# Kernel optimization log

Hardware: AMD Instinct MI355X
Metric: run time of the kernel (lower is better)

The kernel has to match this reference:

```python
import jax, jax.numpy as jnp
import numpy as np

B, D, C = 32768, 1024, 40  # batch, proj_dim, num_classes('culture')


def setup_inputs() -> dict:
    key = jax.random.key(0)
    k1, k2, k3, k4, k5 = jax.random.split(key, 5)
    scale = 1.0 / np.sqrt(D)
    return {
        "src": jax.random.normal(k1, (B, D), dtype=jnp.float32),
        "attn_mask": jnp.ones((B,), dtype=jnp.float32),  # unpacked but unused by BiChain
        # padded weights: row i uses only first D+i columns; the rest hit zero buffer slots
        "W": jax.random.normal(k2, (C, D + C), dtype=jnp.float32) * scale,
        "b": jax.random.normal(k3, (C,), dtype=jnp.float32) * scale,
        "W_rev": jax.random.normal(k4, (C, D + C), dtype=jnp.float32) * scale,
        "b_rev": jax.random.normal(k5, (C,), dtype=jnp.float32) * scale,
    }


def _chain(src, W, b):
    """Sequential classifier chain: score_i = sigmoid(<[src, s_0..s_{i-1}], w_i> + b_i)."""
    Bsz, Df = src.shape
    Cn = W.shape[0]
    # growing feature buffer, pre-padded with zeros for future scores
    buf0 = jnp.zeros((Bsz, Df + Cn), dtype=src.dtype).at[:, :Df].set(src)

    def step(buf, inp):
        w_i, b_i, i = inp
        score = jax.nn.sigmoid(buf @ w_i + b_i)            # [B]
        buf = jax.lax.dynamic_update_slice(buf, score[:, None], (0, Df + i))
        return buf, score

    _, scores = jax.lax.scan(step, buf0, (W, b, jnp.arange(Cn)))
    return scores.T  # [B, C]


def reference(src, attn_mask, W, b, W_rev, b_rev):
    out_fwd = _chain(src, W, b)
    out_rev = _chain(src, W_rev, b_rev)
    return (out_fwd + out_rev[:, ::-1]) * 0.5
```

## Files before the change

kernel.cpp:

```cpp
#include <hip/hip_runtime.h>
#include <hip/hip_bf16.h>
#include <math.h>

using short8   = __attribute__((ext_vector_type(8))) short;
using ushort4v = __attribute__((ext_vector_type(4))) unsigned short;
using float4v  = __attribute__((ext_vector_type(4))) float;

#define D_DIM 1024
#define NCLS  40
#define WSTR  1064
#define TM    64
#define NCH   16

__device__ __forceinline__ short f2bf(float f) {
    __hip_bfloat16 h = __float2bfloat16(f);
    union { __hip_bfloat16 h; short s; } u; u.h = h;
    return u.s;
}

__global__ void convert_w_kernel(const float* __restrict__ W, const float* __restrict__ Wr,
                                 short* __restrict__ Wfrag) {
    int idx  = blockIdx.x * 256 + threadIdx.x;
    int lane = idx & 63;
    int rest = idx >> 6;
    int t    = rest % 5;
    int rest2 = rest / 5;
    int ks   = rest2 & 1;
    int ch   = rest2 >> 1;
    int cls  = t * 16 + (lane & 15);
    int k0   = ch * 64 + ks * 32 + (lane >> 4) * 8;
    const float* srow = (cls < NCLS) ? (W + (size_t)cls * WSTR)
                                     : (Wr + (size_t)(cls - NCLS) * WSTR);
    short8 v;
#pragma unroll
    for (int e = 0; e < 8; ++e) v[e] = f2bf(srow[k0 + e]);
    *(short8*)(Wfrag + (size_t)idx * 8) = v;
}

__global__ __launch_bounds__(256, 2) void bichain_main(
    const float* __restrict__ src, const short* __restrict__ Wfrag,
    const float* __restrict__ Wf, const float* __restrict__ Wr,
    const float* __restrict__ bf_, const float* __restrict__ br_,
    float* __restrict__ out)
{
    __shared__ __align__(16) char smem[24576];

    const int tid  = threadIdx.x;
    const int lane = tid & 63;
    const int wave = tid >> 6;
    const int row0 = blockIdx.x * TM;
    const int i16  = lane & 15;
    const int i4   = lane >> 4;

    char* ldsW = smem + wave * 6144;
    const float* aGlob = src + (size_t)(row0 + wave * 16 + i4) * D_DIM + i16 * 4;

    float4v ap[3][4];
    short8  wp[2][10];
    float4v acc[5];
#pragma unroll
    for (int t = 0; t < 5; ++t)
#pragma unroll
        for (int r = 0; r < 4; ++r) acc[t][r] = 0.f;

#define LOADA(ch) do { if ((ch) < NCH) {                                   \
    const float* _p = aGlob + (ch) * 64;                                   \
    ap[(ch)%3][0] = *(const float4v*)(_p);                                 \
    ap[(ch)%3][1] = *(const float4v*)(_p + 4 * D_DIM);                     \
    ap[(ch)%3][2] = *(const float4v*)(_p + 8 * D_DIM);                     \
    ap[(ch)%3][3] = *(const float4v*)(_p + 12 * D_DIM); } } while (0)

#define LOADW(ch) do { if ((ch) < NCH) {                                   \
    const short* _w = Wfrag + (size_t)(ch) * 5120 + (lane << 3);           \
    wp[(ch)%2][0] = *(const short8*)(_w + 0 * 512);                        \
    wp[(ch)%2][1] = *(const short8*)(_w + 1 * 512);                        \
    wp[(ch)%2][2] = *(const short8*)(_w + 2 * 512);                        \
    wp[(ch)%2][3] = *(const short8*)(_w + 3 * 512);                        \
    wp[(ch)%2][4] = *(const short8*)(_w + 4 * 512);                        \
    wp[(ch)%2][5] = *(const short8*)(_w + 5 * 512);                        \
    wp[(ch)%2][6] = *(const short8*)(_w + 6 * 512);                        \
    wp[(ch)%2][7] = *(const short8*)(_w + 7 * 512);                        \
    wp[(ch)%2][8] = *(const short8*)(_w + 8 * 512);                        \
    wp[(ch)%2][9] = *(const short8*)(_w + 9 * 512); } } while (0)

#define DSW1(ch, j) {                                                      \
    int _r = (j) * 4 + i4;                                                 \
    ushort4v _v;                                                           \
    _v[0] = (unsigned short)f2bf(ap[(ch)%3][j][0]);                        \
    _v[1] = (unsigned short)f2bf(ap[(ch)%3][j][1]);                        \
    _v[2] = (unsigned short)f2bf(ap[(ch)%3][j][2]);                        \
    _v[3] = (unsigned short)f2bf(ap[(ch)%3][j][3]);                        \
    *(ushort4v*)(_b + _r * 128 + ((i16 ^ ((_r & 7) << 1)) << 3)) = _v; }
#define DSW(ch) do { if ((ch) < NCH) {                                     \
    char* _b = ldsW + ((ch)%3) * 2048;                                     \
    DSW1(ch, 0) DSW1(ch, 1) DSW1(ch, 2) DSW1(ch, 3) } } while (0)

#define MFMA_(ch) do {                                                     \
    const char* _fb = ldsW + ((ch)%3) * 2048 + i16 * 128;                  \
    const int _sw = (i16 & 7) << 1;                                        \
    short8 _a0 = *(const short8*)(_fb + (((i4 * 2)     ^ _sw) << 3));      \
    acc[0] = __builtin_amdgcn_mfma_f32_16x16x32_bf16(_a0, wp[(ch)%2][0], acc[0], 0, 0, 0); \
    acc[1] = __builtin_amdgcn_mfma_f32_16x16x32_bf16(_a0, wp[(ch)%2][1], acc[1], 0, 0, 0); \
    acc[2] = __builtin_amdgcn_mfma_f32_16x16x32_bf16(_a0, wp[(ch)%2][2], acc[2], 0, 0, 0); \
    acc[3] = __builtin_amdgcn_mfma_f32_16x16x32_bf16(_a0, wp[(ch)%2][3], acc[3], 0, 0, 0); \
    acc[4] = __builtin_amdgcn_mfma_f32_16x16x32_bf16(_a0, wp[(ch)%2][4], acc[4], 0, 0, 0); \
    short8 _a1 = *(const short8*)(_fb + (((8 + i4 * 2) ^ _sw) << 3));      \
    acc[0] = __builtin_amdgcn_mfma_f32_16x16x32_bf16(_a1, wp[(ch)%2][5], acc[0], 0, 0, 0); \
    acc[1] = __builtin_amdgcn_mfma_f32_16x16x32_bf16(_a1, wp[(ch)%2][6], acc[1], 0, 0, 0); \
    acc[2] = __builtin_amdgcn_mfma_f32_16x16x32_bf16(_a1, wp[(ch)%2][7], acc[2], 0, 0, 0); \
    acc[3] = __builtin_amdgcn_mfma_f32_16x16x32_bf16(_a1, wp[(ch)%2][8], acc[3], 0, 0, 0); \
    acc[4] = __builtin_amdgcn_mfma_f32_16x16x32_bf16(_a1, wp[(ch)%2][9], acc[4], 0, 0, 0); \
  } while (0)

#define BODY(ch) do { LOADW((ch)+1); LOADA((ch)+3); DSW((ch)+1); MFMA_(ch); } while (0)

    LOADA(0); LOADA(1); LOADA(2); LOADW(0); DSW(0);
    BODY(0);  BODY(1);  BODY(2);  BODY(3);
    BODY(4);  BODY(5);  BODY(6);  BODY(7);
    BODY(8);  BODY(9);  BODY(10); BODY(11);
    BODY(12); BODY(13); BODY(14); BODY(15);

#undef LOADA
#undef LOADW
#undef DSW1
#undef DSW
#undef MFMA_
#undef BODY

    __syncthreads();

    float* Lg = (float*)smem;
#pragma unroll
    for (int t = 0; t < 5; ++t)
#pragma unroll
        for (int r = 0; r < 4; ++r) {
            int row = wave * 16 + i4 * 4 + r;
            int cls = t * 16 + i16;
            Lg[row * 81 + cls] = acc[t][r];
        }
    __syncthreads();

    if (tid < 128) {
        const int row = tid >> 1;
        const int dir = tid & 1;
        const float* Wt = dir ? Wr : Wf;
        const float* bi = dir ? br_ : bf_;
        float s[NCLS];
#pragma unroll
        for (int i = 0; i < NCLS; ++i) {
            float z = Lg[row * 81 + dir * NCLS + i] + bi[i];
#pragma unroll
            for (int j = 0; j < i; ++j)
                z += s[j] * Wt[i * WSTR + D_DIM + j];
            s[i] = 1.f / (1.f + __expf(-z));
            Lg[row * 81 + dir * NCLS + i] = s[i];
        }
    }
    __syncthreads();

    float* outp = out + (size_t)row0 * NCLS;
    for (int idx = tid; idx < TM * NCLS; idx += 256) {
        int row = idx / NCLS;
        int c   = idx - row * NCLS;
        outp[idx] = 0.5f * (Lg[row * 81 + c] + Lg[row * 81 + NCLS + (NCLS - 1 - c)]);
    }
}

extern "C" void kernel_launch(void* const* d_in, const int* in_sizes, int n_in,
                              void* d_out, int out_size, void* d_ws, size_t ws_size,
                              hipStream_t stream) {
    const float* src = (const float*)d_in[0];
    const float* W   = (const float*)d_in[2];
    const float* b   = (const float*)d_in[3];
    const float* Wr  = (const float*)d_in[4];
    const float* br  = (const float*)d_in[5];
    float* out = (float*)d_out;
    short* Wfrag = (short*)d_ws;

    convert_w_kernel<<<40, 256, 0, stream>>>(W, Wr, Wfrag);
    bichain_main<<<512, 256, 0, stream>>>(src, Wfrag, W, Wr, b, br, out);
}
```

Measured before the change: 43.33 us.

## Split GEMM and sequential chain into separate kernels with transposed logits buffer

The fused kernel is split in two. The first does the bf16 MFMA GEMM and writes the logits transposed to a global workspace. The second runs the sequential sigmoid chain with all 256 threads active, one row per thread per direction, reading the chain weights from LDS-staged copies. This removes the serial tail where only 128 of 256 threads ran the 40-step chain with global weight loads inside the GEMM kernel. The cost is an extra kernel launch and a global round trip of the 80xB logits.

```diff
diff --git a/kernel.cpp b/kernel.cpp
--- a/kernel.cpp
+++ b/kernel.cpp
@@ -11,6 +11,7 @@
 #define WSTR  1064
 #define TM    64
 #define NCH   16
+#define BATCH 32768
 
 __device__ __forceinline__ short f2bf(float f) {
     __hip_bfloat16 h = __float2bfloat16(f);
@@ -37,11 +38,9 @@
     *(short8*)(Wfrag + (size_t)idx * 8) = v;
 }
 
-__global__ __launch_bounds__(256, 2) void bichain_main(
+__global__ __launch_bounds__(256, 2) void bichain_gemm(
     const float* __restrict__ src, const short* __restrict__ Wfrag,
-    const float* __restrict__ Wf, const float* __restrict__ Wr,
-    const float* __restrict__ bf_, const float* __restrict__ br_,
-    float* __restrict__ out)
+    float* __restrict__ LgT)
 {
     __shared__ __align__(16) char smem[24576];
 
@@ -127,42 +126,55 @@
 #undef MFMA_
 #undef BODY
 
-    __syncthreads();
-
-    float* Lg = (float*)smem;
 #pragma unroll
     for (int t = 0; t < 5; ++t)
-#pragma unroll
-        for (int r = 0; r < 4; ++r) {
-            int row = wave * 16 + i4 * 4 + r;
-            int cls = t * 16 + i16;
-            Lg[row * 81 + cls] = acc[t][r];
-        }
-    __syncthreads();
+        *(float4v*)(LgT + (size_t)(t * 16 + i16) * BATCH + row0 + wave * 16 + i4 * 4) = acc[t];
+}
 
-    if (tid < 128) {
-        const int row = tid >> 1;
-        const int dir = tid & 1;
+__global__ __launch_bounds__(256) void bichain_chain(
+    const float* __restrict__ LgT,
+    const float* __restrict__ Wf, const float* __restrict__ Wr,
+    const float* __restrict__ bf_, const float* __restrict__ br_,
+    float* __restrict__ out)
+{
+    __shared__ float Tw[2][NCLS][NCLS];
+    __shared__ float Tb[2][NCLS];
+    __shared__ float Sc[128][81];
+
+    const int tid = threadIdx.x;
+    for (int e = tid; e < 2 * NCLS * NCLS; e += 256) {
+        int dir = e / (NCLS * NCLS);
+        int rem = e - dir * (NCLS * NCLS);
+        int i = rem / NCLS, j = rem - i * NCLS;
         const float* Wt = dir ? Wr : Wf;
-        const float* bi = dir ? br_ : bf_;
-        float s[NCLS];
-#pragma unroll
-        for (int i = 0; i < NCLS; ++i) {
-            float z = Lg[row * 81 + dir * NCLS + i] + bi[i];
-#pragma unroll
-            for (int j = 0; j < i; ++j)
-                z += s[j] * Wt[i * WSTR + D_DIM + j];
-            s[i] = 1.f / (1.f + __expf(-z));
-            Lg[row * 81 + dir * NCLS + i] = s[i];
-        }
+        Tw[dir][i][j] = Wt[(size_t)i * WSTR + D_DIM + j];
+    }
+    if (tid < 2 * NCLS) {
+        int dir = tid / NCLS, i = tid - dir * NCLS;
+        Tb[dir][i] = dir ? br_[i] : bf_[i];
     }
     __syncthreads();
 
-    float* outp = out + (size_t)row0 * NCLS;
-    for (int idx = tid; idx < TM * NCLS; idx += 256) {
-        int row = idx / NCLS;
-        int c   = idx - row * NCLS;
-        outp[idx] = 0.5f * (Lg[row * 81 + c] + Lg[row * 81 + NCLS + (NCLS - 1 - c)]);
+    const int rl  = tid & 127;
+    const int dir = tid >> 7;
+    const int row = blockIdx.x * 128 + rl;
+
+    float s[NCLS];
+#pragma unroll
+    for (int i = 0; i < NCLS; ++i) {
+        float z = LgT[(size_t)(dir * NCLS + i) * BATCH + row] + Tb[dir][i];
+#pragma unroll
+        for (int j = 0; j < i; ++j)
+            z += s[j] * Tw[dir][i][j];
+        s[i] = 1.f / (1.f + __expf(-z));
+        Sc[rl][dir * NCLS + i] = s[i];
+    }
+    __syncthreads();
+
+    float* outp = out + (size_t)blockIdx.x * 128 * NCLS;
+    for (int idx = tid; idx < 128 * NCLS; idx += 256) {
+        int r2 = idx / NCLS, c = idx - r2 * NCLS;
+        outp[idx] = 0.5f * (Sc[r2][c] + Sc[r2][NCLS + (NCLS - 1 - c)]);
     }
 }
 
@@ -176,7 +188,9 @@
     const float* br  = (const float*)d_in[5];
     float* out = (float*)d_out;
     short* Wfrag = (short*)d_ws;
+    float* LgT   = (float*)((char*)d_ws + (1 << 20));
 
     convert_w_kernel<<<40, 256, 0, stream>>>(W, Wr, Wfrag);
-    bichain_main<<<512, 256, 0, stream>>>(src, Wfrag, W, Wr, b, br, out);
+    bichain_gemm<<<512, 256, 0, stream>>>(src, Wfrag, LgT);
+    bichain_chain<<<256, 256, 0, stream>>>(LgT, W, Wr, b, br, out);
 }
```

Result: slower. 46.82 us (+8.1%).
